# Kernel optimization log

Hardware: AMD Instinct MI355X
Metric: run time of the kernel (lower is better)

The kernel has to match this reference:

```python
import jax, jax.numpy as jnp
import numpy as np

B, N, DIM, HID = 32, 10000, 64, 128


def _linear_params(key, fan_in, fan_out):
    kw, kb = jax.random.split(key)
    bound = 1.0 / np.sqrt(fan_in)
    w = jax.random.uniform(kw, (fan_out, fan_in), jnp.float32, -bound, bound)
    b = jax.random.uniform(kb, (fan_out,), jnp.float32, -bound, bound)
    return w, b


def setup_inputs() -> dict:
    key = jax.random.key(0)
    ks = jax.random.split(key, 7)
    x = jax.random.normal(ks[0], (B, N, DIM), jnp.float32)
    adj_col = jax.random.uniform(ks[1], (N,), jnp.float32)
    n2e_w, n2e_b = _linear_params(ks[2], 2 * DIM, HID)
    e2e_w, e2e_b = _linear_params(ks[3], HID, HID)
    e2n_w, e2n_b = _linear_params(ks[4], HID, HID)
    n2n_w, n2n_b = _linear_params(ks[5], HID, HID)
    out_w, out_b = _linear_params(ks[6], DIM + HID, DIM)
    return {
        "x": x, "adj_col": adj_col,
        "n2e_w": n2e_w, "n2e_b": n2e_b,
        "e2e_w": e2e_w, "e2e_b": e2e_b,
        "e2n_w": e2n_w, "e2n_b": e2n_b,
        "n2n_w": n2n_w, "n2n_b": n2n_b,
        "out_w": out_w, "out_b": out_b,
        "i": 5, "num": 4, "node_size": 2000,
    }


def reference(x, adj_col, n2e_w, n2e_b, e2e_w, e2e_b, e2n_w, e2n_b,
              n2n_w, n2n_b, out_w, out_b, i, num, node_size):
    # The torch loop over (num+1) chunks is an execution tiling; mathematically it
    # computes a full sum over all N nodes. We vectorize it in one pass.
    starter = x[:, i, :]                                   # [B, dim]
    ender = jnp.broadcast_to(starter[:, None, :], x.shape)  # [B, N, dim]
    c = jnp.concatenate([x, ender], axis=-1)               # [B, N, 2*dim]
    h = jax.nn.relu(jnp.einsum('bnd,hd->bnh', c, n2e_w) + n2e_b)
    h = jax.nn.relu(jnp.einsum('bnh,gh->bng', h, e2e_w) + e2e_b)
    h = h * adj_col[None, :, None]                         # adjacency mask
    s = jnp.sum(h, axis=1)                                 # [B, hid]
    y = jax.nn.relu(s @ e2n_w.T + e2n_b)
    y = jax.nn.relu(y @ n2n_w.T + n2n_b)
    out = jnp.concatenate([starter, y], axis=-1) @ out_w.T + out_b  # [B, dim]
    return out
```

## Files before the change

kernel.cpp:

```cpp
#include <hip/hip_runtime.h>
#include <hip/hip_bf16.h>

typedef float f32x4 __attribute__((ext_vector_type(4)));
typedef short bf16x8 __attribute__((ext_vector_type(8)));
typedef unsigned short u16;
typedef unsigned int u32;

#define NB 32
#define NN 10000
#define DIMX 64

__device__ __forceinline__ u16 f2bf(float f) {
    union { float f; unsigned u; } v; v.f = f;
    unsigned r = (v.u + 0x7FFFu + ((v.u >> 16) & 1u)) >> 16;
    return (u16)r;
}

__device__ __forceinline__ u32 pkbf(float a, float b) {
    __hip_bfloat162 h = __float22bfloat162_rn(make_float2(a, b));
    u32 r; __builtin_memcpy(&r, &h, 4); return r;
}

__global__ void k_prep(const float* __restrict__ x, const float* __restrict__ n2e_w,
                       const float* __restrict__ n2e_b, const float* __restrict__ e2e_w,
                       const int* __restrict__ ip,
                       float* __restrict__ bias1, u16* __restrict__ w1p, u16* __restrict__ w2p) {
    int id = blockIdx.x * 256 + threadIdx.x;
    if (id < 4096) {
        int b = id >> 7, j = id & 127;
        int i = ip[0];
        const float* xr = x + ((size_t)b * NN + i) * DIMX;
        const float* w = n2e_w + j * 128 + 64;
        float s = n2e_b[j];
        #pragma unroll
        for (int d = 0; d < 64; ++d) s += xr[d] * w[d];
        bias1[b * 128 + j] = s;
    } else if (id < 12288) {
        int e = id - 4096;
        int i8 = e & 7, lane = (e >> 3) & 63, kk = (e >> 9) & 1, t = e >> 10;
        int row = t * 16 + (lane & 15), col = kk * 32 + (lane >> 4) * 8 + i8;
        w1p[e] = f2bf(n2e_w[row * 128 + col]);
    } else if (id < 28672) {
        int e = id - 12288;
        int i8 = e & 7, lane = (e >> 3) & 63, kk = (e >> 9) & 3, t = e >> 11;
        int row = t * 16 + (lane & 15), col = kk * 32 + (lane >> 4) * 8 + i8;
        w2p[e] = f2bf(e2e_w[row * 128 + col]);
    }
}

__global__ __launch_bounds__(256, 3) void k_main(
        const float* __restrict__ x, const float* __restrict__ adj,
        const float* __restrict__ bias1, const u16* __restrict__ w1p,
        const u16* __restrict__ w2p, const float* __restrict__ e2e_b,
        float* __restrict__ partials) {
    __shared__ u16 sW1[8192];
    __shared__ u16 sH1[8192];
    __shared__ float sBias[256];
    __shared__ float sAdj[320];

    const int tid = threadIdx.x;
    const int lane = tid & 63, wave = tid >> 6;
    const int c = lane & 15, g = lane >> 4;
    const int bid = blockIdx.x;
    const int b = bid >> 5, qb = bid & 31;
    const int s0 = qb < 17 ? qb * 20 : 340 + (qb - 17) * 19;
    const int cnt = qb < 17 ? 20 : 19;

    #pragma unroll
    for (int p = 0; p < 4; ++p) { int o = (p * 256 + tid) * 8;
        *(bf16x8*)&sW1[o] = *(const bf16x8*)&w1p[o]; }
    if (tid < 128) sBias[tid] = bias1[b * 128 + tid];
    else if (tid < 256) sBias[tid] = e2e_b[tid - 128];
    for (int idx = tid; idx < 320; idx += 256)
        sAdj[idx] = (idx < cnt * 16) ? adj[s0 * 16 + idx] : 0.f;

    const bf16x8* const gW2 = (const bf16x8*)w2p;
    bf16x8 w2r[2][4];
    #pragma unroll
    for (int tt = 0; tt < 2; ++tt)
        #pragma unroll
        for (int kk2 = 0; kk2 < 4; ++kk2)
            w2r[tt][kk2] = gW2[((wave * 2 + tt) * 4 + kk2) * 64 + lane];

    float sAcc[2] = {0.f, 0.f};
    __syncthreads();

    const size_t xbatch = (size_t)b * NN;
    const int swzW = 16 * (c & 3);
    const int rdOff = (c * 64 + 16 * (g ^ (c & 3))) >> 1;

    f32x4 xl[4];
    {
        int idx = wave;
        int stl = idx < cnt ? idx : cnt - 1;
        const float* xr = x + (xbatch + (s0 + stl) * 16 + c) * 64 + g * 8;
        xl[0] = *(const f32x4*)(xr);
        xl[1] = *(const f32x4*)(xr + 4);
        xl[2] = *(const f32x4*)(xr + 32);
        xl[3] = *(const f32x4*)(xr + 36);
    }

    #pragma unroll 1
    for (int it = 0; it < 5; ++it) {
        bf16x8 A1[2];
        #pragma unroll
        for (int kk = 0; kk < 2; ++kk) {
            f32x4 lo = xl[kk * 2], hi = xl[kk * 2 + 1];
            union { bf16x8 v; u32 w[4]; } u;
            u.w[0] = pkbf(lo[0], lo[1]); u.w[1] = pkbf(lo[2], lo[3]);
            u.w[2] = pkbf(hi[0], hi[1]); u.w[3] = pkbf(hi[2], hi[3]);
            A1[kk] = u.v;
        }
        if (it < 4) {
            int idx = (it + 1) * 4 + wave;
            int stl = idx < cnt ? idx : cnt - 1;
            const float* xr = x + (xbatch + (s0 + stl) * 16 + c) * 64 + g * 8;
            xl[0] = *(const f32x4*)(xr);
            xl[1] = *(const f32x4*)(xr + 4);
            xl[2] = *(const f32x4*)(xr + 32);
            xl[3] = *(const f32x4*)(xr + 36);
        }

        u16* const bufW = &sH1[wave * 512];
        #pragma unroll
        for (int kk2 = 0; kk2 < 4; ++kk2) {
            const int t0 = kk2 * 2, t1 = kk2 * 2 + 1;
            bf16x8 w1a0 = *(const bf16x8*)&sW1[(t0 * 2 + 0) * 512 + lane * 8];
            bf16x8 w1b0 = *(const bf16x8*)&sW1[(t0 * 2 + 1) * 512 + lane * 8];
            bf16x8 w1a1 = *(const bf16x8*)&sW1[(t1 * 2 + 0) * 512 + lane * 8];
            bf16x8 w1b1 = *(const bf16x8*)&sW1[(t1 * 2 + 1) * 512 + lane * 8];
            f32x4 cb0 = *(const f32x4*)&sBias[t0 * 16 + 4 * g];
            f32x4 cb1 = *(const f32x4*)&sBias[t1 * 16 + 4 * g];
            f32x4 d0 = __builtin_amdgcn_mfma_f32_16x16x32_bf16(w1a0, A1[0], cb0, 0, 0, 0);
            d0 = __builtin_amdgcn_mfma_f32_16x16x32_bf16(w1b0, A1[1], d0, 0, 0, 0);
            f32x4 d1 = __builtin_amdgcn_mfma_f32_16x16x32_bf16(w1a1, A1[0], cb1, 0, 0, 0);
            d1 = __builtin_amdgcn_mfma_f32_16x16x32_bf16(w1b1, A1[1], d1, 0, 0, 0);
            u32 p00 = pkbf(fmaxf(d0[0], 0.f), fmaxf(d0[1], 0.f));
            u32 p01 = pkbf(fmaxf(d0[2], 0.f), fmaxf(d0[3], 0.f));
            u32 p10 = pkbf(fmaxf(d1[0], 0.f), fmaxf(d1[1], 0.f));
            u32 p11 = pkbf(fmaxf(d1[2], 0.f), fmaxf(d1[3], 0.f));
            int base = c * 64;
            *(uint2*)&bufW[kk2 * 2048 + ((base + ((8 * g) ^ swzW)) >> 1)]      = make_uint2(p00, p01);
            *(uint2*)&bufW[kk2 * 2048 + ((base + ((32 + 8 * g) ^ swzW)) >> 1)] = make_uint2(p10, p11);
        }
        __syncthreads();

        f32x4 acc[4][2];
        #pragma unroll
        for (int sub = 0; sub < 4; ++sub)
            #pragma unroll
            for (int tt = 0; tt < 2; ++tt) acc[sub][tt] = (f32x4){0.f,0.f,0.f,0.f};
        #pragma unroll
        for (int kk2 = 0; kk2 < 4; ++kk2) {
            bf16x8 A2[4];
            #pragma unroll
            for (int sub = 0; sub < 4; ++sub)
                A2[sub] = *(const bf16x8*)&sH1[kk2 * 2048 + sub * 512 + rdOff];
            #pragma unroll
            for (int tt = 0; tt < 2; ++tt)
                #pragma unroll
                for (int sub = 0; sub < 4; ++sub)
                    acc[sub][tt] = __builtin_amdgcn_mfma_f32_16x16x32_bf16(A2[sub], w2r[tt][kk2], acc[sub][tt], 0, 0, 0);
        }
        __syncthreads();

        #pragma unroll
        for (int tt = 0; tt < 2; ++tt) {
            float bb = sBias[128 + (wave * 2 + tt) * 16 + c];
            #pragma unroll
            for (int sub = 0; sub < 4; ++sub) {
                f32x4 av = *(const f32x4*)&sAdj[(it * 4 + sub) * 16 + 4 * g];
                #pragma unroll
                for (int r = 0; r < 4; ++r)
                    sAcc[tt] = fmaf(av[r], fmaxf(acc[sub][tt][r] + bb, 0.f), sAcc[tt]);
            }
        }
    }

    float red[2];
    #pragma unroll
    for (int tt = 0; tt < 2; ++tt) {
        float v = sAcc[tt];
        v += __shfl_xor(v, 16, 64);
        v += __shfl_xor(v, 32, 64);
        red[tt] = v;
    }
    if (lane < 16) {
        #pragma unroll
        for (int tt = 0; tt < 2; ++tt)
            partials[bid * 128 + (wave * 2 + tt) * 16 + lane] = red[tt];
    }
}

__global__ void k_final(const float* __restrict__ partials, const float* __restrict__ x,
                        const int* __restrict__ ip,
                        const float* __restrict__ e2n_w, const float* __restrict__ e2n_b,
                        const float* __restrict__ n2n_w, const float* __restrict__ n2n_b,
                        const float* __restrict__ out_w, const float* __restrict__ out_b,
                        float* __restrict__ out) {
    int b = blockIdx.x, j = threadIdx.x;
    __shared__ float s0[128], s1[128], s2[128];
    float acc = 0.f;
    #pragma unroll
    for (int qq = 0; qq < 32; ++qq) acc += partials[(b * 32 + qq) * 128 + j];
    s0[j] = acc;
    __syncthreads();
    {
        float a1 = e2n_b[j];
        const float* w = e2n_w + j * 128;
        #pragma unroll 8
        for (int k = 0; k < 128; ++k) a1 += w[k] * s0[k];
        s1[j] = fmaxf(a1, 0.f);
    }
    __syncthreads();
    {
        float a2 = n2n_b[j];
        const float* w = n2n_w + j * 128;
        #pragma unroll 8
        for (int k = 0; k < 128; ++k) a2 += w[k] * s1[k];
        s2[j] = fmaxf(a2, 0.f);
    }
    __syncthreads();
    if (j < 64) {
        int i = ip[0];
        const float* xr = x + ((size_t)b * NN + i) * DIMX;
        const float* ow = out_w + j * 192;
        float o = out_b[j];
        #pragma unroll 8
        for (int m = 0; m < 64; ++m) o += ow[m] * xr[m];
        #pragma unroll 8
        for (int m = 0; m < 128; ++m) o += ow[64 + m] * s2[m];
        out[b * 64 + j] = o;
    }
}

extern "C" void kernel_launch(void* const* d_in, const int* in_sizes, int n_in,
                              void* d_out, int out_size, void* d_ws, size_t ws_size,
                              hipStream_t stream) {
    const float* x      = (const float*)d_in[0];
    const float* adj    = (const float*)d_in[1];
    const float* n2e_w  = (const float*)d_in[2];
    const float* n2e_b  = (const float*)d_in[3];
    const float* e2e_w  = (const float*)d_in[4];
    const float* e2e_b  = (const float*)d_in[5];
    const float* e2n_w  = (const float*)d_in[6];
    const float* e2n_b  = (const float*)d_in[7];
    const float* n2n_w  = (const float*)d_in[8];
    const float* n2n_b  = (const float*)d_in[9];
    const float* out_w  = (const float*)d_in[10];
    const float* out_b  = (const float*)d_in[11];
    const int*   ip     = (const int*)d_in[12];
    float* out = (float*)d_out;

    char* ws = (char*)d_ws;
    float* bias1    = (float*)ws;
    u16*   w1p      = (u16*)(ws + 16384);
    u16*   w2p      = (u16*)(ws + 32768);
    float* partials = (float*)(ws + 65536);

    k_prep<<<112, 256, 0, stream>>>(x, n2e_w, n2e_b, e2e_w, ip, bias1, w1p, w2p);
    k_main<<<1024, 256, 0, stream>>>(x, adj, bias1, w1p, w2p, e2e_b, partials);
    k_final<<<32, 128, 0, stream>>>(partials, x, ip, e2n_w, e2n_b, n2n_w, n2n_b,
                                    out_w, out_b, out);
}
```

Baseline: 45.27 us.

## Split layer-1 output features across waves with register-resident W1 and shared X tiles

Layer 1 now partitions output features across waves instead of node tiles. Each wave keeps its slice of W1 and its bias in registers and reads every wave's bf16 X tile from a double-buffered shared array, replacing per-iteration W1 loads from shared memory. The e2e bias moves to registers, and the trailing barrier is removed because the X buffer alternates between iterations. The cost is an extra barrier after the X writes and more register pressure.

```diff
diff --git a/kernel.cpp b/kernel.cpp
--- a/kernel.cpp
+++ b/kernel.cpp
@@ -53,9 +53,9 @@
         const float* __restrict__ bias1, const u16* __restrict__ w1p,
         const u16* __restrict__ w2p, const float* __restrict__ e2e_b,
         float* __restrict__ partials) {
-    __shared__ u16 sW1[8192];
+    __shared__ u16 sX[8192];
     __shared__ u16 sH1[8192];
-    __shared__ float sBias[256];
+    __shared__ float sBias[128];
     __shared__ float sAdj[320];
 
     const int tid = threadIdx.x;
@@ -66,14 +66,15 @@
     const int s0 = qb < 17 ? qb * 20 : 340 + (qb - 17) * 19;
     const int cnt = qb < 17 ? 20 : 19;
 
-    #pragma unroll
-    for (int p = 0; p < 4; ++p) { int o = (p * 256 + tid) * 8;
-        *(bf16x8*)&sW1[o] = *(const bf16x8*)&w1p[o]; }
     if (tid < 128) sBias[tid] = bias1[b * 128 + tid];
-    else if (tid < 256) sBias[tid] = e2e_b[tid - 128];
     for (int idx = tid; idx < 320; idx += 256)
         sAdj[idx] = (idx < cnt * 16) ? adj[s0 * 16 + idx] : 0.f;
 
+    const bf16x8* const gW1 = (const bf16x8*)w1p;
+    const bf16x8 w1a0 = gW1[(wave * 4 + 0) * 64 + lane];
+    const bf16x8 w1b0 = gW1[(wave * 4 + 1) * 64 + lane];
+    const bf16x8 w1a1 = gW1[(wave * 4 + 2) * 64 + lane];
+    const bf16x8 w1b1 = gW1[(wave * 4 + 3) * 64 + lane];
     const bf16x8* const gW2 = (const bf16x8*)w2p;
     bf16x8 w2r[2][4];
     #pragma unroll
@@ -81,9 +82,14 @@
         #pragma unroll
         for (int kk2 = 0; kk2 < 4; ++kk2)
             w2r[tt][kk2] = gW2[((wave * 2 + tt) * 4 + kk2) * 64 + lane];
+    const float b2v0 = e2e_b[(wave * 2 + 0) * 16 + c];
+    const float b2v1 = e2e_b[(wave * 2 + 1) * 16 + c];
 
     float sAcc[2] = {0.f, 0.f};
     __syncthreads();
+
+    const f32x4 cb0 = *(const f32x4*)&sBias[(wave * 2 + 0) * 16 + 4 * g];
+    const f32x4 cb1 = *(const f32x4*)&sBias[(wave * 2 + 1) * 16 + 4 * g];
 
     const size_t xbatch = (size_t)b * NN;
     const int swzW = 16 * (c & 3);
@@ -100,16 +106,16 @@
         xl[3] = *(const f32x4*)(xr + 36);
     }
 
+    int par = 0;
     #pragma unroll 1
     for (int it = 0; it < 5; ++it) {
-        bf16x8 A1[2];
         #pragma unroll
         for (int kk = 0; kk < 2; ++kk) {
             f32x4 lo = xl[kk * 2], hi = xl[kk * 2 + 1];
             union { bf16x8 v; u32 w[4]; } u;
             u.w[0] = pkbf(lo[0], lo[1]); u.w[1] = pkbf(lo[2], lo[3]);
             u.w[2] = pkbf(hi[0], hi[1]); u.w[3] = pkbf(hi[2], hi[3]);
-            A1[kk] = u.v;
+            *(bf16x8*)&sX[(((par * 4 + wave) * 2 + kk) * 64 + lane) * 8] = u.v;
         }
         if (it < 4) {
             int idx = (it + 1) * 4 + wave;
@@ -120,28 +126,24 @@
             xl[2] = *(const f32x4*)(xr + 32);
             xl[3] = *(const f32x4*)(xr + 36);
         }
-
-        u16* const bufW = &sH1[wave * 512];
-        #pragma unroll
-        for (int kk2 = 0; kk2 < 4; ++kk2) {
-            const int t0 = kk2 * 2, t1 = kk2 * 2 + 1;
-            bf16x8 w1a0 = *(const bf16x8*)&sW1[(t0 * 2 + 0) * 512 + lane * 8];
-            bf16x8 w1b0 = *(const bf16x8*)&sW1[(t0 * 2 + 1) * 512 + lane * 8];
-            bf16x8 w1a1 = *(const bf16x8*)&sW1[(t1 * 2 + 0) * 512 + lane * 8];
-            bf16x8 w1b1 = *(const bf16x8*)&sW1[(t1 * 2 + 1) * 512 + lane * 8];
-            f32x4 cb0 = *(const f32x4*)&sBias[t0 * 16 + 4 * g];
-            f32x4 cb1 = *(const f32x4*)&sBias[t1 * 16 + 4 * g];
-            f32x4 d0 = __builtin_amdgcn_mfma_f32_16x16x32_bf16(w1a0, A1[0], cb0, 0, 0, 0);
-            d0 = __builtin_amdgcn_mfma_f32_16x16x32_bf16(w1b0, A1[1], d0, 0, 0, 0);
-            f32x4 d1 = __builtin_amdgcn_mfma_f32_16x16x32_bf16(w1a1, A1[0], cb1, 0, 0, 0);
-            d1 = __builtin_amdgcn_mfma_f32_16x16x32_bf16(w1b1, A1[1], d1, 0, 0, 0);
+        __syncthreads();
+
+        u16* const bufW = &sH1[wave * 2048];
+        #pragma unroll
+        for (int sub = 0; sub < 4; ++sub) {
+            bf16x8 A10 = *(const bf16x8*)&sX[(((par * 4 + sub) * 2 + 0) * 64 + lane) * 8];
+            bf16x8 A11 = *(const bf16x8*)&sX[(((par * 4 + sub) * 2 + 1) * 64 + lane) * 8];
+            f32x4 d0 = __builtin_amdgcn_mfma_f32_16x16x32_bf16(w1a0, A10, cb0, 0, 0, 0);
+            d0 = __builtin_amdgcn_mfma_f32_16x16x32_bf16(w1b0, A11, d0, 0, 0, 0);
+            f32x4 d1 = __builtin_amdgcn_mfma_f32_16x16x32_bf16(w1a1, A10, cb1, 0, 0, 0);
+            d1 = __builtin_amdgcn_mfma_f32_16x16x32_bf16(w1b1, A11, d1, 0, 0, 0);
             u32 p00 = pkbf(fmaxf(d0[0], 0.f), fmaxf(d0[1], 0.f));
             u32 p01 = pkbf(fmaxf(d0[2], 0.f), fmaxf(d0[3], 0.f));
             u32 p10 = pkbf(fmaxf(d1[0], 0.f), fmaxf(d1[1], 0.f));
             u32 p11 = pkbf(fmaxf(d1[2], 0.f), fmaxf(d1[3], 0.f));
             int base = c * 64;
-            *(uint2*)&bufW[kk2 * 2048 + ((base + ((8 * g) ^ swzW)) >> 1)]      = make_uint2(p00, p01);
-            *(uint2*)&bufW[kk2 * 2048 + ((base + ((32 + 8 * g) ^ swzW)) >> 1)] = make_uint2(p10, p11);
+            *(uint2*)&bufW[sub * 512 + ((base + ((8 * g) ^ swzW)) >> 1)]      = make_uint2(p00, p01);
+            *(uint2*)&bufW[sub * 512 + ((base + ((32 + 8 * g) ^ swzW)) >> 1)] = make_uint2(p10, p11);
         }
         __syncthreads();
 
@@ -162,19 +164,17 @@
                 for (int sub = 0; sub < 4; ++sub)
                     acc[sub][tt] = __builtin_amdgcn_mfma_f32_16x16x32_bf16(A2[sub], w2r[tt][kk2], acc[sub][tt], 0, 0, 0);
         }
-        __syncthreads();
-
-        #pragma unroll
-        for (int tt = 0; tt < 2; ++tt) {
-            float bb = sBias[128 + (wave * 2 + tt) * 16 + c];
-            #pragma unroll
-            for (int sub = 0; sub < 4; ++sub) {
-                f32x4 av = *(const f32x4*)&sAdj[(it * 4 + sub) * 16 + 4 * g];
-                #pragma unroll
-                for (int r = 0; r < 4; ++r)
-                    sAcc[tt] = fmaf(av[r], fmaxf(acc[sub][tt][r] + bb, 0.f), sAcc[tt]);
+
+        #pragma unroll
+        for (int sub = 0; sub < 4; ++sub) {
+            f32x4 av = *(const f32x4*)&sAdj[(it * 4 + sub) * 16 + 4 * g];
+            #pragma unroll
+            for (int r = 0; r < 4; ++r) {
+                sAcc[0] = fmaf(av[r], fmaxf(acc[sub][0][r] + b2v0, 0.f), sAcc[0]);
+                sAcc[1] = fmaf(av[r], fmaxf(acc[sub][1][r] + b2v1, 0.f), sAcc[1]);
             }
         }
+        par ^= 1;
     }
 
     float red[2];
```

Result: faster. 43.58 us (-3.7%).
